# Optimization experiments

Hardware: AMD Instinct MI355X
Metric: run time of the kernel (lower is better)

The kernel has to match this reference:

```python
import jax, jax.numpy as jnp
import numpy as np

NUM_HEADS = 8
OUT_CH = 64
IN_CH = 512
N_NODES = 65536


def setup_inputs() -> dict:
    key = jax.random.key(0)
    ks = jax.random.split(key, 8)
    s = 1.0 / np.sqrt(IN_CH)
    return {
        "query_input": jax.random.normal(ks[0], (N_NODES, IN_CH), jnp.float32),
        "source_input": jax.random.normal(ks[1], (N_NODES, IN_CH), jnp.float32),
        "Wq_w": jax.random.normal(ks[2], (NUM_HEADS * OUT_CH, IN_CH), jnp.float32) * s,
        "Wq_b": jax.random.normal(ks[3], (NUM_HEADS * OUT_CH,), jnp.float32) * s,
        "Wk_w": jax.random.normal(ks[4], (NUM_HEADS * OUT_CH, IN_CH), jnp.float32) * s,
        "Wk_b": jax.random.normal(ks[5], (NUM_HEADS * OUT_CH,), jnp.float32) * s,
        "Wv_w": jax.random.normal(ks[6], (NUM_HEADS * OUT_CH, IN_CH), jnp.float32) * s,
        "Wv_b": jax.random.normal(ks[7], (NUM_HEADS * OUT_CH,), jnp.float32) * s,
    }


def reference(query_input, source_input, Wq_w, Wq_b, Wk_w, Wk_b, Wv_w, Wv_b):
    N = query_input.shape[0]
    # Linear projections (torch nn.Linear: x @ W^T + b), reshape to [N, H, D]
    qs = (query_input @ Wq_w.T + Wq_b).reshape(N, NUM_HEADS, OUT_CH)
    ks = (source_input @ Wk_w.T + Wk_b).reshape(N, NUM_HEADS, OUT_CH)
    vs = (source_input @ Wv_w.T + Wv_b).reshape(N, NUM_HEADS, OUT_CH)
    # GLOBAL Frobenius-norm normalization (torch.norm with no dim)
    qs = qs / jnp.linalg.norm(qs)
    ks = ks / jnp.linalg.norm(ks)
    Nf = jnp.asarray(N, qs.dtype)
    # Global KV aggregation: [H, D, D]
    kvs = jnp.einsum('lhm,lhd->hmd', ks, vs)
    attention_num = jnp.einsum('nhm,hmd->nhd', qs, kvs) + Nf * vs
    ks_sum = ks.sum(axis=0)  # [H, D]
    attention_normalizer = jnp.einsum('nhm,hm->nh', qs, ks_sum)[..., None] + Nf
    attn_output = attention_num / attention_normalizer  # [N, H, D]
    return attn_output.mean(axis=1)  # [N, D]
```

## Files before the change

### kernel.cpp

```cpp
#include <hip/hip_runtime.h>
#include <stdint.h>

typedef __attribute__((ext_vector_type(8))) short short8;
typedef __attribute__((ext_vector_type(4))) float f32x4;

__device__ __forceinline__ uint32_t pk2bf(float a, float b) {
  uint32_t r;
  asm("v_cvt_pk_bf16_f32 %0, %1, %2" : "=v"(r) : "v"(a), "v"(b));
  return r;
}
__device__ __forceinline__ uint16_t f2bf(float a) {
  uint32_t ua = __builtin_bit_cast(uint32_t, a);
  return (uint16_t)((ua + 0x7FFFu + ((ua >> 16) & 1u)) >> 16);
}
__device__ __forceinline__ float bflo(uint32_t w) { return __builtin_bit_cast(float, w << 16); }
__device__ __forceinline__ float bfhi(uint32_t w) { return __builtin_bit_cast(float, w & 0xFFFF0000u); }

__device__ __forceinline__ void gload_lds16(const void* g, void* l) {
  __builtin_amdgcn_global_load_lds(
      (const __attribute__((address_space(1))) uint32_t*)g,
      (__attribute__((address_space(3))) uint32_t*)l, 16, 0, 0);
}

__global__ __launch_bounds__(256) void k_cvtw(const float* __restrict__ Wq,
                                              const float* __restrict__ Wk,
                                              const float* __restrict__ Wv,
                                              uint16_t* __restrict__ Wb) {
  const int idx = blockIdx.x * 256 + threadIdx.x;
  const int sel = idx >> 16;
  const int e = idx & 65535;
  const float* src = (sel == 0) ? Wq : (sel == 1) ? Wk : Wv;
  const float4 v = *(const float4*)(src + (size_t)e * 4);
  uint2 p;
  p.x = pk2bf(v.x, v.y);
  p.y = pk2bf(v.z, v.w);
  *(uint2*)(Wb + (size_t)sel * 262144 + (size_t)e * 4) = p;
}

__global__ __launch_bounds__(256, 3) void k_gemm_qkv(
    const float* __restrict__ qin, const float* __restrict__ sin_,
    const uint16_t* __restrict__ Wb,
    const float* __restrict__ bq, const float* __restrict__ bk,
    const float* __restrict__ bv,
    uint16_t* __restrict__ Qb, uint16_t* __restrict__ Kb, uint16_t* __restrict__ Vb,
    float* __restrict__ norms, float* __restrict__ ks_sum) {
  __shared__ float Asf[128 * 64];
  __shared__ uint16_t Bs[128 * 64];
  __shared__ float ksp[128];
  __shared__ float red[4];

  const int b0 = blockIdx.x;
  const int blk = (b0 & 7) * 768 + (b0 >> 3);
  const int rt = blk / 12, rem = blk % 12;
  const int proj = rem >> 2, ct = rem & 3;
  const int row0 = rt * 128, cb = ct * 128;

  const float* A = proj ? sin_ : qin;
  const uint16_t* W = Wb + (size_t)proj * 262144;
  const float* Bi = (proj == 0) ? bq : (proj == 1) ? bk : bv;
  uint16_t* O = (proj == 0) ? Qb : (proj == 1) ? Kb : Vb;

  const int tid = threadIdx.x;
  const int lane = tid & 63;
  const int wv = tid >> 6;
  const int wr = wv >> 1, wc = wv & 1;
  const int l15 = lane & 15, lhi = lane >> 4;

  f32x4 acc[4][4];
#pragma unroll
  for (int m = 0; m < 4; ++m)
#pragma unroll
    for (int n = 0; n < 4; ++n) acc[m][n] = (f32x4){0.f, 0.f, 0.f, 0.f};

  for (int kt = 0; kt < 8; ++kt) {
    const int k0 = kt * 64;
#pragma unroll
    for (int i = 0; i < 8; ++i) {
      const int arow = (wv * 8 + i) * 4 + (lane >> 4);
      const int ac16 = (lane & 15) ^ (arow & 7);
      gload_lds16(A + (size_t)(row0 + arow) * 512 + k0 + ac16 * 4,
                  &Asf[(wv * 8 + i) * 256]);
    }
#pragma unroll
    for (int i = 0; i < 4; ++i) {
      const int brow = (wv * 4 + i) * 8 + (lane >> 3);
      const int bc16 = (lane & 7) ^ (brow & 7);
      gload_lds16(W + (size_t)(cb + brow) * 512 + k0 + bc16 * 8,
                  &Bs[(wv * 4 + i) * 512]);
    }
    __syncthreads();
#pragma unroll
    for (int kk = 0; kk < 2; ++kk) {
      short8 a[4], b[4];
#pragma unroll
      for (int m = 0; m < 4; ++m) {
        const int r = wr * 64 + m * 16 + l15;
        const int base = r * 256 + kk * 128 + lhi * 32;
        const int sw = (r & 7) << 4;
        const f32x4 f0 = *(const f32x4*)((const char*)Asf + (base ^ sw));
        const f32x4 f1 = *(const f32x4*)((const char*)Asf + ((base + 16) ^ sw));
        uint32_t* ap = (uint32_t*)&a[m];
        ap[0] = pk2bf(f0[0], f0[1]);
        ap[1] = pk2bf(f0[2], f0[3]);
        ap[2] = pk2bf(f1[0], f1[1]);
        ap[3] = pk2bf(f1[2], f1[3]);
      }
#pragma unroll
      for (int n = 0; n < 4; ++n) {
        const int c = wc * 64 + n * 16 + l15;
        const int bo = (c * 128 + kk * 64 + lhi * 16) ^ ((c & 7) << 4);
        b[n] = *(const short8*)((const char*)Bs + bo);
      }
#pragma unroll
      for (int m = 0; m < 4; ++m)
#pragma unroll
        for (int n = 0; n < 4; ++n)
          acc[m][n] = __builtin_amdgcn_mfma_f32_16x16x32_bf16(a[m], b[n], acc[m][n], 0, 0, 0);
    }
    __syncthreads();
  }

  float nrm = 0.f;
  float cs[4] = {0.f, 0.f, 0.f, 0.f};
#pragma unroll
  for (int n = 0; n < 4; ++n) {
    const int colg = cb + wc * 64 + n * 16 + l15;
    const float bias = Bi[colg];
#pragma unroll
    for (int m = 0; m < 4; ++m) {
      const int rowb = row0 + wr * 64 + m * 16 + lhi * 4;
#pragma unroll
      for (int r = 0; r < 4; ++r) {
        const float v = acc[m][n][r] + bias;
        O[(size_t)(rowb + r) * 512 + colg] = f2bf(v);
        nrm += v * v;
        cs[n] += v;
      }
    }
  }
#pragma unroll
  for (int o = 32; o >= 1; o >>= 1) nrm += __shfl_xor(nrm, o, 64);
  if (lane == 0) red[wv] = nrm;
  if (tid < 128) ksp[tid] = 0.f;
  __syncthreads();
  if (proj == 1) {
#pragma unroll
    for (int n = 0; n < 4; ++n) {
      cs[n] += __shfl_xor(cs[n], 16, 64);
      cs[n] += __shfl_xor(cs[n], 32, 64);
    }
    if (lhi == 0) {
#pragma unroll
      for (int n = 0; n < 4; ++n) atomicAdd(&ksp[wc * 64 + n * 16 + l15], cs[n]);
    }
  }
  __syncthreads();
  if (tid == 0 && proj < 2)
    atomicAdd(&norms[proj], red[0] + red[1] + red[2] + red[3]);
  if (proj == 1 && tid < 128) atomicAdd(&ks_sum[cb + tid], ksp[tid]);
}

__global__ __launch_bounds__(256) void k_kvs(const uint16_t* __restrict__ Kb,
                                             const uint16_t* __restrict__ Vb,
                                             float* __restrict__ part) {
  __shared__ uint16_t Ks[64 * 128];
  __shared__ uint16_t Vs[64 * 128];
  const int tid = threadIdx.x;
  const int hp = blockIdx.x & 3;
  const int chunk = blockIdx.x >> 2;
  const int tm = tid >> 4, td = tid & 15;
  float acc0[4][4], acc1[4][4];
#pragma unroll
  for (int a = 0; a < 4; ++a)
#pragma unroll
    for (int b = 0; b < 4; ++b) { acc0[a][b] = 0.f; acc1[a][b] = 0.f; }

  for (int nb = 0; nb < 16; ++nb) {
    const int n0 = chunk * 1024 + nb * 64;
#pragma unroll
    for (int i = 0; i < 4; ++i) {
      const int id = i * 256 + tid;
      const int row = id >> 4, c8 = id & 15;
      *(uint4*)(&Ks[row * 128 + c8 * 8]) =
          *(const uint4*)(Kb + (size_t)(n0 + row) * 512 + hp * 128 + c8 * 8);
      *(uint4*)(&Vs[row * 128 + c8 * 8]) =
          *(const uint4*)(Vb + (size_t)(n0 + row) * 512 + hp * 128 + c8 * 8);
    }
    __syncthreads();
    for (int nn = 0; nn < 64; ++nn) {
      const uint2 kw0 = *(const uint2*)(&Ks[nn * 128 + tm * 4]);
      const uint2 kw1 = *(const uint2*)(&Ks[nn * 128 + 64 + tm * 4]);
      const uint2 vw0 = *(const uint2*)(&Vs[nn * 128 + td * 4]);
      const uint2 vw1 = *(const uint2*)(&Vs[nn * 128 + 64 + td * 4]);
      const float km0[4] = {bflo(kw0.x), bfhi(kw0.x), bflo(kw0.y), bfhi(kw0.y)};
      const float km1[4] = {bflo(kw1.x), bfhi(kw1.x), bflo(kw1.y), bfhi(kw1.y)};
      const float vd0[4] = {bflo(vw0.x), bfhi(vw0.x), bflo(vw0.y), bfhi(vw0.y)};
      const float vd1[4] = {bflo(vw1.x), bfhi(vw1.x), bflo(vw1.y), bfhi(vw1.y)};
#pragma unroll
      for (int a = 0; a < 4; ++a)
#pragma unroll
        for (int b = 0; b < 4; ++b) {
          acc0[a][b] = fmaf(km0[a], vd0[b], acc0[a][b]);
          acc1[a][b] = fmaf(km1[a], vd1[b], acc1[a][b]);
        }
    }
    __syncthreads();
  }
  float* p = part + (size_t)chunk * 32768 + (size_t)hp * 128 * 64;
#pragma unroll
  for (int a = 0; a < 4; ++a)
#pragma unroll
    for (int b = 0; b < 4; ++b) {
      p[(tm * 4 + a) * 64 + td * 4 + b] = acc0[a][b];
      p[(64 + tm * 4 + a) * 64 + td * 4 + b] = acc1[a][b];
    }
}

__global__ __launch_bounds__(256) void k_kvsT(const float* __restrict__ part,
                                              uint16_t* __restrict__ kvsT) {
  const int id = blockIdx.x * 256 + threadIdx.x;
  const int k = id >> 6, d = id & 63;
  float s0 = 0.f, s1 = 0.f, s2 = 0.f, s3 = 0.f;
#pragma unroll
  for (int c = 0; c < 64; c += 4) {
    s0 += part[(size_t)(c + 0) * 32768 + id];
    s1 += part[(size_t)(c + 1) * 32768 + id];
    s2 += part[(size_t)(c + 2) * 32768 + id];
    s3 += part[(size_t)(c + 3) * 32768 + id];
  }
  kvsT[(size_t)d * 512 + k] = f2bf((s0 + s1) + (s2 + s3));
}

__global__ __launch_bounds__(256, 2) void k_num(const uint16_t* __restrict__ Qb,
                                                const uint16_t* __restrict__ Vb,
                                                const uint16_t* __restrict__ kvsT,
                                                const float* __restrict__ ks_sum,
                                                const float* __restrict__ norms,
                                                float* __restrict__ out) {
  __shared__ uint16_t KT[64 * 512];
  __shared__ float kss[512];
  __shared__ float aS[128 * 8];
  __shared__ float bS[128 * 8];
  const int tid = threadIdx.x, lane = tid & 63, wv = tid >> 6;
  const int l15 = lane & 15, lhi = lane >> 4;
  const int row0 = blockIdx.x * 128;

#pragma unroll
  for (int i = 0; i < 16; ++i) {
    const int d = wv * 16 + i;
    const int sc = lane ^ (d & 7);
    gload_lds16(kvsT + (size_t)d * 512 + sc * 8, &KT[d * 512]);
  }
  kss[tid] = ks_sum[tid];
  kss[tid + 256] = ks_sum[tid + 256];
  __syncthreads();
  const float scale = 1.0f / (sqrtf(norms[0]) * sqrtf(norms[1]));

  {
    const int r = tid >> 1, h0 = (tid & 1) * 4;
#pragma unroll
    for (int hh = 0; hh < 4; ++hh) {
      const int h = h0 + hh;
      const uint16_t* q = Qb + (size_t)(row0 + r) * 512 + h * 64;
      const float* ks = &kss[h * 64];
      float dot = 0.f;
#pragma unroll
      for (int i = 0; i < 8; ++i) {
        const uint4 w = *(const uint4*)(q + i * 8);
        const uint32_t dw[4] = {w.x, w.y, w.z, w.w};
#pragma unroll
        for (int c = 0; c < 4; ++c) {
          dot = fmaf(bflo(dw[c]), ks[i * 8 + c * 2], dot);
          dot = fmaf(bfhi(dw[c]), ks[i * 8 + c * 2 + 1], dot);
        }
      }
      const float den = fmaf(scale, dot, 65536.0f);
      aS[r * 8 + h] = scale / (8.0f * den);
      bS[r * 8 + h] = 8192.0f / den;
    }
  }
  __syncthreads();

  short8 If[2][4];
#pragma unroll
  for (int kk = 0; kk < 2; ++kk)
#pragma unroll
    for (int n = 0; n < 4; ++n) {
      const int pos = n * 16 + l15 - kk * 32 - lhi * 8;
      uint32_t* p = (uint32_t*)&If[kk][n];
#pragma unroll
      for (int jw = 0; jw < 4; ++jw)
        p[jw] = ((pos >> 1) == jw) ? ((pos & 1) ? 0x3F800000u : 0x00003F80u) : 0u;
    }

  f32x4 acc[2][4];
#pragma unroll
  for (int m = 0; m < 2; ++m)
#pragma unroll
    for (int n = 0; n < 4; ++n) acc[m][n] = (f32x4){0.f, 0.f, 0.f, 0.f};

  for (int h = 0; h < 8; ++h) {
#pragma unroll
    for (int kk = 0; kk < 2; ++kk) {
      short8 bfr[4];
#pragma unroll
      for (int n = 0; n < 4; ++n) {
        const int d = n * 16 + l15;
        const int bo = (d * 1024 + h * 128 + kk * 64 + lhi * 16) ^ ((d & 7) << 4);
        bfr[n] = *(const short8*)((const char*)KT + bo);
      }
#pragma unroll
      for (int m = 0; m < 2; ++m) {
        const int r = wv * 32 + m * 16 + l15;
        const float sc = aS[r * 8 + h];
        const uint4 w =
            *(const uint4*)(Qb + (size_t)(row0 + r) * 512 + h * 64 + kk * 32 + lhi * 8);
        const uint32_t dw[4] = {w.x, w.y, w.z, w.w};
        short8 af;
        uint32_t* ap = (uint32_t*)&af;
#pragma unroll
        for (int c = 0; c < 4; ++c) ap[c] = pk2bf(bflo(dw[c]) * sc, bfhi(dw[c]) * sc);
#pragma unroll
        for (int n = 0; n < 4; ++n)
          acc[m][n] = __builtin_amdgcn_mfma_f32_16x16x32_bf16(af, bfr[n], acc[m][n], 0, 0, 0);
      }
    }
  }
  for (int h = 0; h < 8; ++h) {
#pragma unroll
    for (int kk = 0; kk < 2; ++kk) {
#pragma unroll
      for (int m = 0; m < 2; ++m) {
        const int r = wv * 32 + m * 16 + l15;
        const float sc = bS[r * 8 + h];
        const uint4 w =
            *(const uint4*)(Vb + (size_t)(row0 + r) * 512 + h * 64 + kk * 32 + lhi * 8);
        const uint32_t dw[4] = {w.x, w.y, w.z, w.w};
        short8 af;
        uint32_t* ap = (uint32_t*)&af;
#pragma unroll
        for (int c = 0; c < 4; ++c) ap[c] = pk2bf(bflo(dw[c]) * sc, bfhi(dw[c]) * sc);
#pragma unroll
        for (int n = 0; n < 4; ++n)
          acc[m][n] = __builtin_amdgcn_mfma_f32_16x16x32_bf16(af, If[kk][n], acc[m][n], 0, 0, 0);
      }
    }
  }

#pragma unroll
  for (int m = 0; m < 2; ++m)
#pragma unroll
    for (int n = 0; n < 4; ++n)
#pragma unroll
      for (int j = 0; j < 4; ++j)
        out[(size_t)(row0 + wv * 32 + m * 16 + lhi * 4 + j) * 64 + n * 16 + l15] =
            acc[m][n][j];
}

extern "C" void kernel_launch(void* const* d_in, const int* in_sizes, int n_in,
                              void* d_out, int out_size, void* d_ws, size_t ws_size,
                              hipStream_t stream) {
  const float* qin = (const float*)d_in[0];
  const float* sin_ = (const float*)d_in[1];
  const float* Wq = (const float*)d_in[2];
  const float* bq = (const float*)d_in[3];
  const float* Wk = (const float*)d_in[4];
  const float* bk = (const float*)d_in[5];
  const float* Wv = (const float*)d_in[6];
  const float* bv = (const float*)d_in[7];
  float* out = (float*)d_out;

  char* ws = (char*)d_ws;
  float* ks_sum = (float*)ws;
  float* norms = (float*)(ws + 2048);
  uint16_t* kvsT = (uint16_t*)(ws + 4096);
  uint16_t* Wb = (uint16_t*)(ws + 69632);
  uint16_t* Qb = (uint16_t*)(ws + (2ull << 20));
  uint16_t* Kb = (uint16_t*)(ws + (2ull << 20) + 67108864ull);
  uint16_t* Vb = (uint16_t*)(ws + (2ull << 20) + 134217728ull);
  float* part = (float*)(ws + 194ull * 1048576ull);

  hipMemsetAsync(d_ws, 0, 2056, stream);

  k_cvtw<<<dim3(768), dim3(256), 0, stream>>>(Wq, Wk, Wv, Wb);
  k_gemm_qkv<<<dim3(6144), dim3(256), 0, stream>>>(qin, sin_, Wb, bq, bk, bv,
                                                   Qb, Kb, Vb, norms, ks_sum);
  k_kvs<<<dim3(256), dim3(256), 0, stream>>>(Kb, Vb, part);
  k_kvsT<<<dim3(128), dim3(256), 0, stream>>>(part, kvsT);
  k_num<<<dim3(512), dim3(256), 0, stream>>>(Qb, Vb, kvsT, ks_sum, norms, out);
}
```

Before: 346.3 us.

## Double-buffer QKV GEMM LDS tiles with K=32 stages to overlap loads and MFMA

Turns the single-buffered K=64 tile loop of the QKV projection GEMM into a double-buffered K=32 pipeline. The next stage's global->LDS loads are issued before computing on the current buffer, with a partial vmcnt wait and raw barriers. The goal is to hide global load latency behind MFMA work. LDS size stays the same, but there are twice as many iterations and barriers, and a new swizzle for the B tile.

```diff
diff --git a/kernel.cpp b/kernel.cpp
--- a/kernel.cpp
+++ b/kernel.cpp
@@ -44,8 +44,8 @@
     const float* __restrict__ bv,
     uint16_t* __restrict__ Qb, uint16_t* __restrict__ Kb, uint16_t* __restrict__ Vb,
     float* __restrict__ norms, float* __restrict__ ks_sum) {
-  __shared__ float Asf[128 * 64];
-  __shared__ uint16_t Bs[128 * 64];
+  __shared__ float Asf[2][128 * 32];
+  __shared__ uint16_t Bs[2][128 * 32];
   __shared__ float ksp[128];
   __shared__ float red[4];
 
@@ -72,52 +72,73 @@
 #pragma unroll
     for (int n = 0; n < 4; ++n) acc[m][n] = (f32x4){0.f, 0.f, 0.f, 0.f};
 
-  for (int kt = 0; kt < 8; ++kt) {
-    const int k0 = kt * 64;
-#pragma unroll
-    for (int i = 0; i < 8; ++i) {
-      const int arow = (wv * 8 + i) * 4 + (lane >> 4);
-      const int ac16 = (lane & 15) ^ (arow & 7);
-      gload_lds16(A + (size_t)(row0 + arow) * 512 + k0 + ac16 * 4,
-                  &Asf[(wv * 8 + i) * 256]);
-    }
+  auto stage = [&](int buf, int kt) {
+    const int k0 = kt * 32;
 #pragma unroll
     for (int i = 0; i < 4; ++i) {
-      const int brow = (wv * 4 + i) * 8 + (lane >> 3);
-      const int bc16 = (lane & 7) ^ (brow & 7);
-      gload_lds16(W + (size_t)(cb + brow) * 512 + k0 + bc16 * 8,
-                  &Bs[(wv * 4 + i) * 512]);
-    }
-    __syncthreads();
-#pragma unroll
-    for (int kk = 0; kk < 2; ++kk) {
-      short8 a[4], b[4];
-#pragma unroll
-      for (int m = 0; m < 4; ++m) {
-        const int r = wr * 64 + m * 16 + l15;
-        const int base = r * 256 + kk * 128 + lhi * 32;
-        const int sw = (r & 7) << 4;
-        const f32x4 f0 = *(const f32x4*)((const char*)Asf + (base ^ sw));
-        const f32x4 f1 = *(const f32x4*)((const char*)Asf + ((base + 16) ^ sw));
-        uint32_t* ap = (uint32_t*)&a[m];
-        ap[0] = pk2bf(f0[0], f0[1]);
-        ap[1] = pk2bf(f0[2], f0[3]);
-        ap[2] = pk2bf(f1[0], f1[1]);
-        ap[3] = pk2bf(f1[2], f1[3]);
-      }
-#pragma unroll
-      for (int n = 0; n < 4; ++n) {
-        const int c = wc * 64 + n * 16 + l15;
-        const int bo = (c * 128 + kk * 64 + lhi * 16) ^ ((c & 7) << 4);
-        b[n] = *(const short8*)((const char*)Bs + bo);
-      }
-#pragma unroll
-      for (int m = 0; m < 4; ++m)
-#pragma unroll
-        for (int n = 0; n < 4; ++n)
-          acc[m][n] = __builtin_amdgcn_mfma_f32_16x16x32_bf16(a[m], b[n], acc[m][n], 0, 0, 0);
-    }
-    __syncthreads();
+      const int ii = wv * 4 + i;
+      const int r = ii * 8 + (lane >> 3);
+      const int ch = (lane & 7) ^ (r & 7);
+      gload_lds16(A + (size_t)(row0 + r) * 512 + k0 + ch * 4,
+                  &Asf[buf][ii * 256]);
+    }
+#pragma unroll
+    for (int i = 0; i < 2; ++i) {
+      const int ii = wv * 2 + i;
+      const int s = ii * 64 + lane;
+      const int c = s >> 2, chp = s & 3;
+      const int k8 = chp ^ ((c >> 1) & 3);
+      gload_lds16(W + (size_t)(cb + c) * 512 + k0 + k8 * 8,
+                  &Bs[buf][ii * 512]);
+    }
+  };
+
+  stage(0, 0);
+  asm volatile("s_waitcnt vmcnt(0)" ::: "memory");
+  __builtin_amdgcn_s_barrier();
+  __builtin_amdgcn_sched_barrier(0);
+
+  int cur = 0;
+  for (int kt = 0; kt < 16; ++kt) {
+    if (kt < 15) {
+      stage(cur ^ 1, kt + 1);
+      asm volatile("s_waitcnt vmcnt(6)" ::: "memory");
+    } else {
+      asm volatile("s_waitcnt vmcnt(0)" ::: "memory");
+    }
+    __builtin_amdgcn_s_barrier();
+    __builtin_amdgcn_sched_barrier(0);
+
+    short8 a[4], b[4];
+#pragma unroll
+    for (int m = 0; m < 4; ++m) {
+      const int r = wr * 64 + m * 16 + l15;
+      const int off = r * 128 + lhi * 32;
+      const int sw = (r & 7) << 4;
+      const char* base = (const char*)Asf[cur];
+      const f32x4 f0 = *(const f32x4*)(base + (off ^ sw));
+      const f32x4 f1 = *(const f32x4*)(base + ((off + 16) ^ sw));
+      uint32_t* ap = (uint32_t*)&a[m];
+      ap[0] = pk2bf(f0[0], f0[1]);
+      ap[1] = pk2bf(f0[2], f0[3]);
+      ap[2] = pk2bf(f1[0], f1[1]);
+      ap[3] = pk2bf(f1[2], f1[3]);
+    }
+#pragma unroll
+    for (int n = 0; n < 4; ++n) {
+      const int c = wc * 64 + n * 16 + l15;
+      const int off = c * 64 + ((lhi ^ ((c >> 1) & 3)) * 16);
+      b[n] = *(const short8*)((const char*)Bs[cur] + off);
+    }
+#pragma unroll
+    for (int m = 0; m < 4; ++m)
+#pragma unroll
+      for (int n = 0; n < 4; ++n)
+        acc[m][n] = __builtin_amdgcn_mfma_f32_16x16x32_bf16(a[m], b[n], acc[m][n], 0, 0, 0);
+
+    __builtin_amdgcn_sched_barrier(0);
+    __builtin_amdgcn_s_barrier();
+    cur ^= 1;
   }
 
   float nrm = 0.f;
```

Measured after the change: 386.5 us. 11.6% more time.

## Convert A tile to bf16 in registers before LDS store, halving LDS footprint

Applied to the files above, without the earlier changes.

The A operand tile was previously copied into LDS as fp32 via direct global-to-LDS loads and converted to bf16 on every fragment read. It is now loaded into registers, converted to bf16 once, and written to a swizzled bf16 LDS tile, so MFMA fragments are read with one 16-byte load. This halves A's LDS usage, which allows raising the occupancy hint from 3 to 4 blocks per CU. The trade-off is that the async global_load_lds path is replaced by synchronous register loads plus LDS stores, which adds VGPR pressure and load latency that the warps must hide.

```diff
diff --git a/kernel.cpp b/kernel.cpp
--- a/kernel.cpp
+++ b/kernel.cpp
@@ -37,14 +37,14 @@
   *(uint2*)(Wb + (size_t)sel * 262144 + (size_t)e * 4) = p;
 }
 
-__global__ __launch_bounds__(256, 3) void k_gemm_qkv(
+__global__ __launch_bounds__(256, 4) void k_gemm_qkv(
     const float* __restrict__ qin, const float* __restrict__ sin_,
     const uint16_t* __restrict__ Wb,
     const float* __restrict__ bq, const float* __restrict__ bk,
     const float* __restrict__ bv,
     uint16_t* __restrict__ Qb, uint16_t* __restrict__ Kb, uint16_t* __restrict__ Vb,
     float* __restrict__ norms, float* __restrict__ ks_sum) {
-  __shared__ float Asf[128 * 64];
+  __shared__ uint16_t As[128 * 64];
   __shared__ uint16_t Bs[128 * 64];
   __shared__ float ksp[128];
   __shared__ float red[4];
@@ -75,11 +75,28 @@
   for (int kt = 0; kt < 8; ++kt) {
     const int k0 = kt * 64;
 #pragma unroll
-    for (int i = 0; i < 8; ++i) {
-      const int arow = (wv * 8 + i) * 4 + (lane >> 4);
-      const int ac16 = (lane & 15) ^ (arow & 7);
-      gload_lds16(A + (size_t)(row0 + arow) * 512 + k0 + ac16 * 4,
-                  &Asf[(wv * 8 + i) * 256]);
+    for (int half = 0; half < 2; ++half) {
+      const int c0 = (half * 2) * 256 + tid;
+      const int c1 = (half * 2 + 1) * 256 + tid;
+      const int r0 = c0 >> 3, e0 = c0 & 7;
+      const int r1 = c1 >> 3, e1 = c1 & 7;
+      const float* s0 = A + (size_t)(row0 + r0) * 512 + k0 + e0 * 8;
+      const float* s1 = A + (size_t)(row0 + r1) * 512 + k0 + e1 * 8;
+      const float4 v00 = *(const float4*)s0;
+      const float4 v01 = *(const float4*)(s0 + 4);
+      const float4 v10 = *(const float4*)s1;
+      const float4 v11 = *(const float4*)(s1 + 4);
+      uint4 w0, w1;
+      w0.x = pk2bf(v00.x, v00.y);
+      w0.y = pk2bf(v00.z, v00.w);
+      w0.z = pk2bf(v01.x, v01.y);
+      w0.w = pk2bf(v01.z, v01.w);
+      w1.x = pk2bf(v10.x, v10.y);
+      w1.y = pk2bf(v10.z, v10.w);
+      w1.z = pk2bf(v11.x, v11.y);
+      w1.w = pk2bf(v11.z, v11.w);
+      *(uint4*)((char*)As + (size_t)(r0 * 8 + (e0 ^ (r0 & 7))) * 16) = w0;
+      *(uint4*)((char*)As + (size_t)(r1 * 8 + (e1 ^ (r1 & 7))) * 16) = w1;
     }
 #pragma unroll
     for (int i = 0; i < 4; ++i) {
@@ -95,15 +112,8 @@
 #pragma unroll
       for (int m = 0; m < 4; ++m) {
         const int r = wr * 64 + m * 16 + l15;
-        const int base = r * 256 + kk * 128 + lhi * 32;
-        const int sw = (r & 7) << 4;
-        const f32x4 f0 = *(const f32x4*)((const char*)Asf + (base ^ sw));
-        const f32x4 f1 = *(const f32x4*)((const char*)Asf + ((base + 16) ^ sw));
-        uint32_t* ap = (uint32_t*)&a[m];
-        ap[0] = pk2bf(f0[0], f0[1]);
-        ap[1] = pk2bf(f0[2], f0[3]);
-        ap[2] = pk2bf(f1[0], f1[1]);
-        ap[3] = pk2bf(f1[2], f1[3]);
+        const int bo = (r * 128 + kk * 64 + lhi * 16) ^ ((r & 7) << 4);
+        a[m] = *(const short8*)((const char*)As + bo);
       }
 #pragma unroll
       for (int n = 0; n < 4; ++n) {
```

New measurement: 404.5 us. 16.8% more time.
